# Kernel tuning notes

Measured on AMD Instinct MI355X. Metric: run time of the kernel, lower is better.

The kernel has to match this reference:

```python
import jax, jax.numpy as jnp
import numpy as np

# ---- static config (matches init_kwargs) ----
B, S, D = 2, 4096, 1024          # batch, seq_len, dim_input
L, ST = 512, 64                  # segment_len, state_len
H = 8                            # num_heads
DK0, DV0, DK1, DV1 = 64, 64, 64, 64  # per-head key/value dims for 2 memory levels
DH = 4096                        # dim_hidden (MLP)
T = 2 * ST + L                   # tokens per segment block: [state, segment, state]


def setup_inputs() -> dict:
    key = jax.random.key(0)
    ks = jax.random.split(key, 18)
    f32 = jnp.float32
    def w(k, shape, fan_in):
        return (jax.random.normal(k, shape, dtype=f32) / np.float32(np.sqrt(fan_in)))
    return {
        "x": jax.random.normal(ks[0], (B, S, D), dtype=f32),
        "state_init": 0.02 * jax.random.normal(ks[1], (ST, D), dtype=f32),
        # level-0 projections: dim_input -> per-head (key/value)
        "Wq0": w(ks[2], (D, H, DK0), D),
        "Wk0": w(ks[3], (D, H, DK0), D),
        "Wv0": w(ks[4], (D, H, DV0), D),
        # level-1 projections: level-0 value dim -> per-head (key/value)
        "Wq1": w(ks[5], (H, DV0, DK1), DV0),
        "Wk1": w(ks[6], (H, DV0, DK1), DV0),
        "Wv1": w(ks[7], (H, DV0, DV1), DV0),
        # output projection back to dim_input
        "Wo": w(ks[8], (H, DV1, D), H * DV1),
        "bo": jnp.zeros((D,), f32),
        "g_attn": jnp.ones((D,), f32),
        "b_attn": jnp.zeros((D,), f32),
        "W1": w(ks[9], (D, DH), D),
        "b1": jnp.zeros((DH,), f32),
        "W2": w(ks[10], (DH, D), DH),
        "b2": jnp.zeros((D,), f32),
        "g_mlp": jnp.ones((D,), f32),
        "b_mlp": jnp.zeros((D,), f32),
    }


def _layernorm(x, g, b, eps=1e-5):
    mu = jnp.mean(x, axis=-1, keepdims=True)
    var = jnp.mean(jnp.square(x - mu), axis=-1, keepdims=True)
    return (x - mu) * jax.lax.rsqrt(var + eps) * g + b


def _rope(x, pos):
    # x: (B, H, T, dk); rotary embedding with base 10000
    dk = x.shape[-1]
    inv_freq = jnp.power(jnp.float32(10000.0), -jnp.arange(0, dk, 2, dtype=jnp.float32) / dk)
    ang = pos[:, None] * inv_freq[None, :]              # (T, dk/2)
    cos, sin = jnp.cos(ang), jnp.sin(ang)
    x1, x2 = x[..., 0::2], x[..., 1::2]
    r1 = x1 * cos - x2 * sin
    r2 = x1 * sin + x2 * cos
    return jnp.stack([r1, r2], axis=-1).reshape(x.shape)


def _attend(q, k, v, mask):
    # q,k: (B,H,T,dk); v: (B,H,T,dv); causal mask (T,T)
    scale = jnp.float32(1.0 / np.sqrt(q.shape[-1]))
    scores = jnp.einsum('bhqc,bhkc->bhqk', q, k) * scale
    scores = jnp.where(mask, scores, jnp.float32(-1e30))
    p = jax.nn.softmax(scores, axis=-1)
    return jnp.einsum('bhqk,bhkv->bhqv', p, v)


def _remmtas(x, state_init, Wq0, Wk0, Wv0, Wq1, Wk1, Wv1, Wo, bo):
    b, s, d = x.shape
    n_seg = s // L
    xs = x.reshape(b, n_seg, L, d).transpose(1, 0, 2, 3)   # (n_seg, B, L, D)
    mask = jnp.tril(jnp.ones((T, T), dtype=bool))
    pos = jnp.arange(T, dtype=jnp.float32)
    state0 = jnp.broadcast_to(state_init, (b, ST, d))

    def step(state, seg):
        toks = jnp.concatenate([state, seg, state], axis=1)      # (B, T, D)
        # memory level 0
        q0 = _rope(jnp.einsum('btd,dhk->bhtk', toks, Wq0), pos)
        k0 = _rope(jnp.einsum('btd,dhk->bhtk', toks, Wk0), pos)
        v0 = jnp.einsum('btd,dhv->bhtv', toks, Wv0)
        o0 = _attend(q0, k0, v0, mask)                           # (B,H,T,DV0)
        # memory level 1 (consumes level-0 values, per-head)
        q1 = _rope(jnp.einsum('bhtv,hvk->bhtk', o0, Wq1), pos)
        k1 = _rope(jnp.einsum('bhtv,hvk->bhtk', o0, Wk1), pos)
        v1 = jnp.einsum('bhtv,hvw->bhtw', o0, Wv1)
        o1 = _attend(q1, k1, v1, mask)                           # (B,H,T,DV1)
        out = jnp.einsum('bhtv,hvd->btd', o1, Wo) + bo           # (B,T,D)
        new_state = out[:, ST + L:]                              # trailing state tokens
        return new_state, out[:, ST:ST + L]                      # segment output

    _, outs = jax.lax.scan(step, state0, xs)                     # (n_seg, B, L, D)
    return outs.transpose(1, 0, 2, 3).reshape(b, s, d)


def reference(x, state_init, Wq0, Wk0, Wv0, Wq1, Wk1, Wv1, Wo, bo,
              g_attn, b_attn, W1, b1, W2, b2, g_mlp, b_mlp):
    a = _remmtas(x, state_init, Wq0, Wk0, Wv0, Wq1, Wk1, Wv1, Wo, bo)
    h = _layernorm(a + x, g_attn, b_attn)
    m = jax.nn.gelu(h @ W1 + b1, approximate=False) @ W2 + b2
    # note: second residual adds the ORIGINAL x, per the source code
    return _layernorm(m + x, g_mlp, b_mlp)
```

## Files before the change

### kernel.cpp

```cpp
#include <hip/hip_runtime.h>
#include <hip/hip_bf16.h>

typedef __hip_bfloat16 bf16;
typedef short bf16x8 __attribute__((ext_vector_type(8)));
typedef float f32x4 __attribute__((ext_vector_type(4)));

#define CB 2
#define CS 4096
#define CD 1024
#define CL 512
#define CST 64
#define CH 8
#define CT 640
#define CDH 4096
#define NSEG 8
#define MCH 2048
#define LP 80

__device__ __forceinline__ float tof(float x) { return x; }
__device__ __forceinline__ float tof(bf16 x) { return __bfloat162float(x); }
__device__ __forceinline__ void storev(float* p, float v) { *p = v; }
__device__ __forceinline__ void storev(bf16* p, float v) { *p = __float2bfloat16(v); }

__device__ __forceinline__ float ldin(const void* p, size_t i, int f32w) {
    if (f32w) return ((const float*)p)[i];
    return __bfloat162float(((const bf16*)p)[i]);
}

__global__ void sniff_kernel(const void* x, int* flag) {
    if (threadIdx.x == 0 && blockIdx.x == 0) {
        const bf16* hb = (const bf16*)x;
        int plaus = 0;
        for (int i = 0; i < 256; ++i) {
            float v = __bfloat162float(hb[2 * i]);
            float a = fabsf(v);
            if (v == 0.f || (a > 1e-4f && a < 100.f)) ++plaus;
        }
        flag[0] = (plaus < 128) ? 1 : 0;
    }
}

__global__ __launch_bounds__(256) void transpose_kernel(
    const void* __restrict__ in, bf16* __restrict__ out, int R, int C,
    const int* __restrict__ flag)
{
    const int f32w = flag[0];
    __shared__ short t[64][72];
    int tid = threadIdx.x;
    int c0 = blockIdx.x * 64, r0 = blockIdx.y * 64;
    int cc = tid & 63, rr = tid >> 6;
#pragma unroll
    for (int i = 0; i < 16; ++i) {
        bf16 v = __float2bfloat16(ldin(in, (size_t)(r0 + rr + i * 4) * C + c0 + cc, f32w));
        t[rr + i * 4][cc] = *(short*)&v;
    }
    __syncthreads();
#pragma unroll
    for (int i = 0; i < 16; ++i)
        ((short*)out)[(size_t)(c0 + rr + i * 4) * R + r0 + cc] = t[cc][rr + i * 4];
}

__global__ __launch_bounds__(256) void transpose3_kernel(
    const void* __restrict__ in0, const void* __restrict__ in1, const void* __restrict__ in2,
    bf16* __restrict__ out0, bf16* __restrict__ out1, bf16* __restrict__ out2,
    const int* __restrict__ flag)
{
    const int f32w = flag[0];
    const void* in = (blockIdx.z == 0) ? in0 : (blockIdx.z == 1 ? in1 : in2);
    bf16* out = (blockIdx.z == 0) ? out0 : (blockIdx.z == 1 ? out1 : out2);
    const int R = CD, C = 512;
    __shared__ short t[64][72];
    int tid = threadIdx.x;
    int c0 = blockIdx.x * 64, r0 = blockIdx.y * 64;
    int cc = tid & 63, rr = tid >> 6;
#pragma unroll
    for (int i = 0; i < 16; ++i) {
        bf16 v = __float2bfloat16(ldin(in, (size_t)(r0 + rr + i * 4) * C + c0 + cc, f32w));
        t[rr + i * 4][cc] = *(short*)&v;
    }
    __syncthreads();
#pragma unroll
    for (int i = 0; i < 16; ++i)
        ((short*)out)[(size_t)(c0 + rr + i * 4) * R + r0 + cc] = t[cc][rr + i * 4];
}

__global__ __launch_bounds__(256) void transposeH_kernel(
    const void* __restrict__ Wq1, const void* __restrict__ Wk1, const void* __restrict__ Wv1,
    bf16* __restrict__ oq, bf16* __restrict__ ok, bf16* __restrict__ ov,
    const int* __restrict__ flag)
{
    const int f32w = flag[0];
    int which = blockIdx.x >> 3, hh = blockIdx.x & 7;
    const void* in = (which == 0) ? Wq1 : (which == 1) ? Wk1 : Wv1;
    bf16* out = (which == 0) ? oq : (which == 1) ? ok : ov;
    __shared__ short t[64][72];
    int tid = threadIdx.x;
    int cc = tid & 63, rr = tid >> 6;
    size_t base = (size_t)hh * 4096;
#pragma unroll
    for (int i = 0; i < 16; ++i) {
        bf16 v = __float2bfloat16(ldin(in, base + (size_t)(rr + i * 4) * 64 + cc, f32w));
        t[rr + i * 4][cc] = *(short*)&v;
    }
    __syncthreads();
#pragma unroll
    for (int i = 0; i < 16; ++i)
        ((short*)out)[base + (size_t)(rr + i * 4) * 64 + cc] = t[cc][rr + i * 4];
}

template <typename TC, int ACT, int OUTM>
__global__ __launch_bounds__(256) void mfma_lds(
    const bf16* __restrict__ A,
    const bf16* __restrict__ Bt0, const bf16* __restrict__ Bt1, const bf16* __restrict__ Bt2,
    TC* __restrict__ C0, TC* __restrict__ C1, TC* __restrict__ C2,
    const void* __restrict__ bias, int M, int N, int K, int seg,
    const int* __restrict__ flag)
{
    const int f32w = flag[0];
    const bf16* Bt = (blockIdx.z == 0) ? Bt0 : (blockIdx.z == 1 ? Bt1 : Bt2);
    TC* C = (blockIdx.z == 0) ? C0 : (blockIdx.z == 1 ? C1 : C2);

    __shared__ __align__(16) short As[128 * 64];
    __shared__ __align__(16) short Bs[128 * 64];

    const int tid = threadIdx.x;
    const int lane = tid & 63;
    const int w = tid >> 6;
    const int wm = w >> 1, wn = w & 1;
    const int bm = blockIdx.x * 128, bn = blockIdx.y * 128;

    f32x4 acc[4][4];
#pragma unroll
    for (int i = 0; i < 4; ++i)
#pragma unroll
        for (int j = 0; j < 4; ++j) acc[i][j] = (f32x4){0.f, 0.f, 0.f, 0.f};

    int srow[4], skc[4];
#pragma unroll
    for (int i = 0; i < 4; ++i) {
        int c = i * 256 + tid;
        srow[i] = c >> 3;
        skc[i] = (c & 7) * 8;
    }

    bf16x8 rA0[4], rB0[4], rA1[4], rB1[4];
#pragma unroll
    for (int i = 0; i < 4; ++i) {
        rA0[i] = *(const bf16x8*)(A + (size_t)(bm + srow[i]) * K + skc[i]);
        rB0[i] = *(const bf16x8*)(Bt + (size_t)(bn + srow[i]) * K + skc[i]);
        rA1[i] = *(const bf16x8*)(A + (size_t)(bm + srow[i]) * K + 64 + skc[i]);
        rB1[i] = *(const bf16x8*)(Bt + (size_t)(bn + srow[i]) * K + 64 + skc[i]);
    }

#define MFMA_PHASE                                                              \
    _Pragma("unroll")                                                           \
    for (int kh = 0; kh < 2; ++kh) {                                            \
        bf16x8 av[4], bv[4];                                                    \
        _Pragma("unroll")                                                       \
        for (int mi = 0; mi < 4; ++mi) {                                        \
            int r = wm * 64 + mi * 16 + (lane & 15);                            \
            int cl = kh * 4 + (lane >> 4);                                      \
            av[mi] = *(const bf16x8*)&As[r * 64 + cl * 8];                      \
        }                                                                       \
        _Pragma("unroll")                                                       \
        for (int nj = 0; nj < 4; ++nj) {                                        \
            int r = wn * 64 + nj * 16 + (lane & 15);                            \
            int cl = kh * 4 + (lane >> 4);                                      \
            bv[nj] = *(const bf16x8*)&Bs[r * 64 + cl * 8];                      \
        }                                                                       \
        _Pragma("unroll")                                                       \
        for (int mi = 0; mi < 4; ++mi)                                          \
            _Pragma("unroll")                                                   \
            for (int nj = 0; nj < 4; ++nj)                                      \
                acc[mi][nj] = __builtin_amdgcn_mfma_f32_16x16x32_bf16(          \
                    av[mi], bv[nj], acc[mi][nj], 0, 0, 0);                      \
    }

    for (int k0 = 0; k0 < K; k0 += 128) {
        __syncthreads();
#pragma unroll
        for (int i = 0; i < 4; ++i) {
            *(bf16x8*)&As[(size_t)(i * 256 + tid) * 8] = rA0[i];
            *(bf16x8*)&Bs[(size_t)(i * 256 + tid) * 8] = rB0[i];
        }
        if (k0 + 128 < K) {
            int kn = k0 + 128;
#pragma unroll
            for (int i = 0; i < 4; ++i) {
                rA0[i] = *(const bf16x8*)(A + (size_t)(bm + srow[i]) * K + kn + skc[i]);
                rB0[i] = *(const bf16x8*)(Bt + (size_t)(bn + srow[i]) * K + kn + skc[i]);
            }
        }
        __syncthreads();
        MFMA_PHASE

        __syncthreads();
#pragma unroll
        for (int i = 0; i < 4; ++i) {
            *(bf16x8*)&As[(size_t)(i * 256 + tid) * 8] = rA1[i];
            *(bf16x8*)&Bs[(size_t)(i * 256 + tid) * 8] = rB1[i];
        }
        if (k0 + 192 < K) {
            int kn = k0 + 192;
#pragma unroll
            for (int i = 0; i < 4; ++i) {
                rA1[i] = *(const bf16x8*)(A + (size_t)(bm + srow[i]) * K + kn + skc[i]);
                rB1[i] = *(const bf16x8*)(Bt + (size_t)(bn + srow[i]) * K + kn + skc[i]);
            }
        }
        __syncthreads();
        MFMA_PHASE
    }
#undef MFMA_PHASE

#pragma unroll
    for (int mi = 0; mi < 4; ++mi) {
#pragma unroll
        for (int nj = 0; nj < 4; ++nj) {
            int c = bn + wn * 64 + nj * 16 + (lane & 15);
            float bia = bias ? ldin(bias, c, f32w) : 0.f;
#pragma unroll
            for (int r = 0; r < 4; ++r) {
                int row = bm + wm * 64 + mi * 16 + (lane >> 4) * 4 + r;
                float v = acc[mi][nj][r] + bia;
                if (ACT == 1) v = 0.5f * v * (1.0f + erff(v * 0.70710678118654752f));
                if (OUTM == 0) {
                    storev(C + (size_t)row * N + c, v);
                } else {
                    int bb2 = row / CT, t = row % CT;
                    if (t >= CST) {
                        if (t < CST + CL)
                            storev(C0 + ((size_t)bb2 * CS + (size_t)seg * CL + (t - CST)) * CD + c, v);
                        else
                            storev(C1 + ((size_t)bb2 * CST + (t - CST - CL)) * CD + c, v);
                    }
                }
            }
        }
    }
}

__global__ __launch_bounds__(256) void ropeV_kernel(
    bf16* __restrict__ q, bf16* __restrict__ k,
    const bf16* __restrict__ v, bf16* __restrict__ vt)
{
    int t0 = blockIdx.x * 64, hh = blockIdx.y, b = blockIdx.z;
    int tid = threadIdx.x;
    __shared__ short lt[64][72];
    int c = tid & 63;
    int r0 = tid >> 6;
    int ip = c >> 1;
    float inv = powf(10000.f, -(float)(2 * ip) / 64.f);
#pragma unroll
    for (int i = 0; i < 16; ++i) {
        int r = r0 + i * 4;
        int t = t0 + r;
        size_t idx = ((size_t)b * CT + t) * 512 + hh * 64 + c;
        float qv = tof(q[idx]);
        float kv = tof(k[idx]);
        float ang = (float)t * inv;
        float sn, cs;
        sincosf(ang, &sn, &cs);
        float qp = __shfl_xor(qv, 1);
        float kp = __shfl_xor(kv, 1);
        float rq, rk;
        if (c & 1) { rq = qp * sn + qv * cs; rk = kp * sn + kv * cs; }
        else       { rq = qv * cs - qp * sn; rk = kv * cs - kp * sn; }
        q[idx] = __float2bfloat16(rq);
        k[idx] = __float2bfloat16(rk);
        lt[r][c] = ((const short*)v)[idx];
    }
    __syncthreads();
#pragma unroll
    for (int i = 0; i < 16; ++i) {
        int c2 = r0 + i * 4;
        int r2 = c;
        ((short*)vt)[((size_t)(b * CH + hh) * 64 + c2) * CT + t0 + r2] = lt[r2][c2];
    }
}

template <int FUSE>
__global__ __launch_bounds__(256) void attn_mfma(
    const bf16* __restrict__ q, const bf16* __restrict__ k, const bf16* __restrict__ vt,
    bf16* __restrict__ o,
    int qsb, int qsh, int qst,
    int ksb, int ksh, int kst,
    int ob, int oh, int ot,
    const bf16* __restrict__ Wq1t, const bf16* __restrict__ Wk1t, const bf16* __restrict__ Wv1t,
    bf16* __restrict__ q1o, bf16* __restrict__ k1o, bf16* __restrict__ v1to)
{
    const int tid = threadIdx.x;
    const int lane = tid & 63;
    const int wrow = tid >> 6;
    const int hh = blockIdx.y, b = blockIdx.z;
    const int qbase = ((int)gridDim.x - 1 - (int)blockIdx.x) * 64;

    __shared__ __align__(16) short Qs[64 * LP];
    __shared__ __align__(16) short Ks[64 * LP];
    __shared__ __align__(16) short Vs[64 * LP];
    __shared__ __align__(16) short Ps[64 * LP];

    const size_t qb0 = (size_t)b * qsb + (size_t)hh * qsh;
    const size_t kb0 = (size_t)b * ksb + (size_t)hh * ksh;
    const size_t vtb = (size_t)(b * CH + hh) * 64 * CT;

    int srow[2], skc[2], soff[2];
#pragma unroll
    for (int i = 0; i < 2; ++i) {
        int c = i * 256 + tid;
        srow[i] = c >> 3;
        skc[i] = c & 7;
        soff[i] = srow[i] * LP + skc[i] * 8;
    }

    bf16x8 rQ[2], rK[2], rV[2];
#pragma unroll
    for (int i = 0; i < 2; ++i) {
        rQ[i] = *(const bf16x8*)(q + qb0 + (size_t)(qbase + srow[i]) * qst + skc[i] * 8);
        rK[i] = *(const bf16x8*)(k + kb0 + (size_t)srow[i] * kst + skc[i] * 8);
        rV[i] = *(const bf16x8*)(vt + vtb + (size_t)srow[i] * CT + skc[i] * 8);
    }

    float mrow[4], lrow[4];
    f32x4 oacc[4];
#pragma unroll
    for (int r = 0; r < 4; ++r) { mrow[r] = -1e30f; lrow[r] = 0.f; }
#pragma unroll
    for (int nd = 0; nd < 4; ++nd) oacc[nd] = (f32x4){0.f, 0.f, 0.f, 0.f};

    const int ntiles = qbase / 64 + 1;
    for (int ti = 0; ti < ntiles; ++ti) {
        __syncthreads();
        if (ti == 0) {
#pragma unroll
            for (int i = 0; i < 2; ++i) *(bf16x8*)&Qs[soff[i]] = rQ[i];
        }
#pragma unroll
        for (int i = 0; i < 2; ++i) {
            *(bf16x8*)&Ks[soff[i]] = rK[i];
            *(bf16x8*)&Vs[soff[i]] = rV[i];
        }
        if (ti + 1 < ntiles) {
            int j1 = (ti + 1) * 64;
#pragma unroll
            for (int i = 0; i < 2; ++i) {
                rK[i] = *(const bf16x8*)(k + kb0 + (size_t)(j1 + srow[i]) * kst + skc[i] * 8);
                rV[i] = *(const bf16x8*)(vt + vtb + (size_t)srow[i] * CT + j1 + skc[i] * 8);
            }
        }
        __syncthreads();

        f32x4 sacc[4];
#pragma unroll
        for (int nj = 0; nj < 4; ++nj) sacc[nj] = (f32x4){0.f, 0.f, 0.f, 0.f};
#pragma unroll
        for (int kh = 0; kh < 2; ++kh) {
            int cl = kh * 4 + (lane >> 4);
            bf16x8 av = *(const bf16x8*)&Qs[(wrow * 16 + (lane & 15)) * LP + cl * 8];
#pragma unroll
            for (int nj = 0; nj < 4; ++nj) {
                bf16x8 bv = *(const bf16x8*)&Ks[(nj * 16 + (lane & 15)) * LP + cl * 8];
                sacc[nj] = __builtin_amdgcn_mfma_f32_16x16x32_bf16(av, bv, sacc[nj], 0, 0, 0);
            }
        }

        const bool diag = (ti == ntiles - 1);
        float pm[4] = {-1e30f, -1e30f, -1e30f, -1e30f};
#pragma unroll
        for (int nj = 0; nj < 4; ++nj) {
            int col_l = nj * 16 + (lane & 15);
#pragma unroll
            for (int r = 0; r < 4; ++r) {
                int row_l = wrow * 16 + ((lane >> 4) << 2) + r;
                float s = (diag && col_l > row_l) ? -1e30f : sacc[nj][r] * 0.125f;
                sacc[nj][r] = s;
                pm[r] = fmaxf(pm[r], s);
            }
        }
#pragma unroll
        for (int msk = 1; msk < 16; msk <<= 1)
#pragma unroll
            for (int r = 0; r < 4; ++r) pm[r] = fmaxf(pm[r], __shfl_xor(pm[r], msk));

        float corr[4], rs[4] = {0.f, 0.f, 0.f, 0.f};
#pragma unroll
        for (int r = 0; r < 4; ++r) {
            float mn = fmaxf(mrow[r], pm[r]);
            corr[r] = __expf(mrow[r] - mn);
            mrow[r] = mn;
        }
#pragma unroll
        for (int nj = 0; nj < 4; ++nj)
#pragma unroll
            for (int r = 0; r < 4; ++r) {
                float p = __expf(sacc[nj][r] - mrow[r]);
                sacc[nj][r] = p;
                rs[r] += p;
            }
#pragma unroll
        for (int msk = 1; msk < 16; msk <<= 1)
#pragma unroll
            for (int r = 0; r < 4; ++r) rs[r] += __shfl_xor(rs[r], msk);
#pragma unroll
        for (int r = 0; r < 4; ++r) lrow[r] = lrow[r] * corr[r] + rs[r];
#pragma unroll
        for (int nd = 0; nd < 4; ++nd)
#pragma unroll
            for (int r = 0; r < 4; ++r) oacc[nd][r] *= corr[r];

#pragma unroll
        for (int nj = 0; nj < 4; ++nj)
#pragma unroll
            for (int r = 0; r < 4; ++r) {
                bf16 pb = __float2bfloat16(sacc[nj][r]);
                Ps[(wrow * 16 + ((lane >> 4) << 2) + r) * LP + nj * 16 + (lane & 15)] =
                    *(short*)&pb;
            }

#pragma unroll
        for (int kh = 0; kh < 2; ++kh) {
            int cl = kh * 4 + (lane >> 4);
            bf16x8 pa = *(const bf16x8*)&Ps[(wrow * 16 + (lane & 15)) * LP + cl * 8];
#pragma unroll
            for (int nd = 0; nd < 4; ++nd) {
                bf16x8 bv = *(const bf16x8*)&Vs[(nd * 16 + (lane & 15)) * LP + cl * 8];
                oacc[nd] = __builtin_amdgcn_mfma_f32_16x16x32_bf16(pa, bv, oacc[nd], 0, 0, 0);
            }
        }
    }

    if (FUSE == 0) {
#pragma unroll
        for (int nd = 0; nd < 4; ++nd) {
#pragma unroll
            for (int r = 0; r < 4; ++r) {
                int row_g = qbase + wrow * 16 + ((lane >> 4) << 2) + r;
                int col = nd * 16 + (lane & 15);
                storev(&o[(size_t)b * ob + (size_t)hh * oh + (size_t)row_g * ot + col],
                       oacc[nd][r] / lrow[r]);
            }
        }
    } else {
#pragma unroll
        for (int nd = 0; nd < 4; ++nd)
#pragma unroll
            for (int r = 0; r < 4; ++r) {
                int row_l = wrow * 16 + ((lane >> 4) << 2) + r;
                bf16 ob16 = __float2bfloat16(oacc[nd][r] / lrow[r]);
                Qs[row_l * LP + nd * 16 + (lane & 15)] = *(short*)&ob16;
            }
        __syncthreads();

        const size_t whb = (size_t)hh * 4096;
        f32x4 qa[4], ka[4], va[4];
#pragma unroll
        for (int nj = 0; nj < 4; ++nj) {
            qa[nj] = (f32x4){0.f, 0.f, 0.f, 0.f};
            ka[nj] = (f32x4){0.f, 0.f, 0.f, 0.f};
            va[nj] = (f32x4){0.f, 0.f, 0.f, 0.f};
        }
#pragma unroll
        for (int kh = 0; kh < 2; ++kh) {
            int cl = kh * 4 + (lane >> 4);
            bf16x8 av = *(const bf16x8*)&Qs[(wrow * 16 + (lane & 15)) * LP + cl * 8];
#pragma unroll
            for (int nj = 0; nj < 4; ++nj) {
                int rowb = nj * 16 + (lane & 15);
                bf16x8 bq = *(const bf16x8*)(Wq1t + whb + (size_t)rowb * 64 + cl * 8);
                bf16x8 bk = *(const bf16x8*)(Wk1t + whb + (size_t)rowb * 64 + cl * 8);
                bf16x8 bw = *(const bf16x8*)(Wv1t + whb + (size_t)rowb * 64 + cl * 8);
                qa[nj] = __builtin_amdgcn_mfma_f32_16x16x32_bf16(av, bq, qa[nj], 0, 0, 0);
                ka[nj] = __builtin_amdgcn_mfma_f32_16x16x32_bf16(av, bk, ka[nj], 0, 0, 0);
                va[nj] = __builtin_amdgcn_mfma_f32_16x16x32_bf16(av, bw, va[nj], 0, 0, 0);
            }
        }
        const size_t bh = (size_t)(b * CH + hh);
#pragma unroll
        for (int nj = 0; nj < 4; ++nj) {
            int col = nj * 16 + (lane & 15);
            int ip = col >> 1;
            float inv = powf(10000.f, -(float)(2 * ip) / 64.f);
#pragma unroll
            for (int r = 0; r < 4; ++r) {
                int row_l = wrow * 16 + ((lane >> 4) << 2) + r;
                int t = qbase + row_l;
                float ang = (float)t * inv;
                float sn, cs;
                sincosf(ang, &sn, &cs);
                float aq = qa[nj][r], ak = ka[nj][r];
                float pq = __shfl_xor(aq, 1);
                float pk = __shfl_xor(ak, 1);
                float rq, rk;
                if (col & 1) { rq = pq * sn + aq * cs; rk = pk * sn + ak * cs; }
                else         { rq = aq * cs - pq * sn; rk = ak * cs - pk * sn; }
                size_t roff = (bh * CT + t) * 64 + col;
                q1o[roff] = __float2bfloat16(rq);
                k1o[roff] = __float2bfloat16(rk);
                v1to[(bh * 64 + col) * CT + t] = __float2bfloat16(va[nj][r]);
            }
        }
    }
}

__global__ __launch_bounds__(256) void build_toks_kernel(
    const void* __restrict__ x, const float* __restrict__ state, bf16* __restrict__ toks,
    int seg, const int* __restrict__ flag)
{
    const int f32w = flag[0];
    int idx = blockIdx.x * 256 + threadIdx.x;
    int d = idx & (CD - 1);
    int t = (idx >> 10) % CT;
    int b = idx / (CT * CD);
    float v;
    if (t < CST) v = state[(b * CST + t) * CD + d];
    else if (t < CST + CL) v = ldin(x, ((size_t)b * CS + seg * CL + (t - CST)) * CD + d, f32w);
    else v = state[(b * CST + (t - CST - CL)) * CD + d];
    toks[idx] = __float2bfloat16(v);
}

__global__ __launch_bounds__(256) void init_state_kernel(
    const void* __restrict__ s0, float* __restrict__ state, const int* __restrict__ flag)
{
    const int f32w = flag[0];
    int idx = blockIdx.x * 256 + threadIdx.x;
    state[idx] = ldin(s0, idx % (CST * CD), f32w);
}

__global__ __launch_bounds__(256) void ln_kernel(
    const float* __restrict__ ra, const void* __restrict__ x,
    const void* __restrict__ g, const void* __restrict__ bb,
    void* __restrict__ outp, int out_ext, const int* __restrict__ flag)
{
    const int f32w = flag[0];
    int row = blockIdx.x;
    int tid = threadIdx.x;
    __shared__ float buf[CD];
    __shared__ float red[4];

    float s = 0.f;
    for (int c = tid; c < CD; c += 256) {
        float v = ra[(size_t)row * CD + c] + ldin(x, (size_t)row * CD + c, f32w);
        buf[c] = v;
        s += v;
    }
#pragma unroll
    for (int off = 32; off; off >>= 1) s += __shfl_xor(s, off);
    if ((tid & 63) == 0) red[tid >> 6] = s;
    __syncthreads();
    float mu = (red[0] + red[1] + red[2] + red[3]) * (1.f / CD);
    __syncthreads();

    float vs = 0.f;
    for (int c = tid; c < CD; c += 256) {
        float d0 = buf[c] - mu;
        vs += d0 * d0;
    }
#pragma unroll
    for (int off = 32; off; off >>= 1) vs += __shfl_xor(vs, off);
    if ((tid & 63) == 0) red[tid >> 6] = vs;
    __syncthreads();
    float var = (red[0] + red[1] + red[2] + red[3]) * (1.f / CD);
    float rs = rsqrtf(var + 1e-5f);

    for (int c = tid; c < CD; c += 256) {
        float y = (buf[c] - mu) * rs * ldin(g, c, f32w) + ldin(bb, c, f32w);
        size_t idx = (size_t)row * CD + c;
        if (!out_ext) {
            ((bf16*)outp)[idx] = __float2bfloat16(y);
        } else if (f32w) {
            ((float*)outp)[idx] = y;
        } else {
            ((bf16*)outp)[idx] = __float2bfloat16(y);
        }
    }
}

extern "C" void kernel_launch(void* const* d_in, const int* in_sizes, int n_in,
                              void* d_out, int out_size, void* d_ws, size_t ws_size,
                              hipStream_t stream)
{
    const void* x      = d_in[0];
    const void* s0     = d_in[1];
    const void* Wq0    = d_in[2];
    const void* Wk0    = d_in[3];
    const void* Wv0    = d_in[4];
    const void* Wq1    = d_in[5];
    const void* Wk1    = d_in[6];
    const void* Wv1    = d_in[7];
    const void* Wo     = d_in[8];
    const void* bo     = d_in[9];
    const void* g_attn = d_in[10];
    const void* b_attn = d_in[11];
    const void* W1     = d_in[12];
    const void* b1     = d_in[13];
    const void* W2     = d_in[14];
    const void* b2     = d_in[15];
    const void* g_mlp  = d_in[16];
    const void* b_mlp  = d_in[17];

    int* flag = (int*)d_ws;
    float* f = (float*)((char*)d_ws + 16);
    float* toks_slot = f; f += (size_t)CB * CT * CD;
    float* q0_slot = f;  f += (size_t)CB * CH * CT * 64;
    float* k0_slot = f;  f += (size_t)CB * CH * CT * 64;
    float* v0_slot = f;  f += (size_t)CB * CH * CT * 64;
    float* o0_slot = f;  f += (size_t)CB * CH * CT * 64;
    float* q1_slot = f;  f += (size_t)CB * CH * CT * 64;
    float* k1_slot = f;  f += (size_t)CB * CH * CT * 64;
    float* v1_slot = f;  f += (size_t)CB * CH * CT * 64;
    float* o1t_slot = f; f += (size_t)CB * CT * (CH * 64);
    float* seg_slot = f; f += (size_t)CB * CT * CD;
    float* state = f;   f += (size_t)CB * CST * CD;
    float* a = f;       f += (size_t)CB * CS * CD;
    bf16* h = (bf16*)f;
    bf16* tail = h + (size_t)CB * CS * CD;

    bf16* toks = (bf16*)toks_slot;
    bf16* q0b = (bf16*)q0_slot;
    bf16* k0b = (bf16*)k0_slot;
    bf16* v0b = (bf16*)v0_slot;
    bf16* v0t = (bf16*)o0_slot;
    bf16* q1b = (bf16*)q1_slot;
    bf16* k1b = (bf16*)k1_slot;
    bf16* v1t = (bf16*)v1_slot;
    bf16* o1t = (bf16*)o1t_slot;
    bf16* WtQ = h;
    bf16* WtK = WtQ + (size_t)512 * 1024;
    bf16* WtV = WtK + (size_t)512 * 1024;
    bf16* WtO = WtV + (size_t)512 * 1024;
    bf16* WtQ1 = WtO + (size_t)1024 * 512;
    bf16* WtK1 = WtQ1 + (size_t)8 * 4096;
    bf16* WtV1 = WtK1 + (size_t)8 * 4096;
    bf16* g1  = (bf16*)toks_slot;
    bf16* Wt1 = g1 + (size_t)MCH * CDH;
    bf16* Wt2 = tail;

    sniff_kernel<<<1, 64, 0, stream>>>(x, flag);
    init_state_kernel<<<(CB * CST * CD) / 256, 256, 0, stream>>>(s0, state, flag);

    transpose3_kernel<<<dim3(8, 16, 3), 256, 0, stream>>>(
        Wq0, Wk0, Wv0, WtQ, WtK, WtV, flag);
    transpose_kernel<<<dim3(16, 8), 256, 0, stream>>>(Wo, WtO, 512, CD, flag);
    transposeH_kernel<<<24, 256, 0, stream>>>(Wq1, Wk1, Wv1, WtQ1, WtK1, WtV1, flag);

    for (int seg = 0; seg < NSEG; ++seg) {
        build_toks_kernel<<<(CB * CT * CD) / 256, 256, 0, stream>>>(x, state, toks, seg, flag);
        mfma_lds<bf16, 0, 0><<<dim3(10, 4, 3), 256, 0, stream>>>(
            toks, WtQ, WtK, WtV, q0b, k0b, v0b, nullptr, CB * CT, 512, CD, 0, flag);
        ropeV_kernel<<<dim3(CT / 64, CH, CB), 256, 0, stream>>>(q0b, k0b, v0b, v0t);
        attn_mfma<1><<<dim3(CT / 64, CH, CB), 256, 0, stream>>>(
            q0b, k0b, v0t, nullptr,
            CT * 512, 64, 512,
            CT * 512, 64, 512,
            0, 0, 0,
            WtQ1, WtK1, WtV1, q1b, k1b, v1t);
        attn_mfma<0><<<dim3(CT / 64, CH, CB), 256, 0, stream>>>(
            q1b, k1b, v1t, o1t,
            CH * CT * 64, CT * 64, 64,
            CH * CT * 64, CT * 64, 64,
            CT * 512, 64, 512,
            nullptr, nullptr, nullptr, nullptr, nullptr, nullptr);
        mfma_lds<float, 0, 1><<<dim3(10, 8, 1), 256, 0, stream>>>(
            o1t, WtO, WtO, WtO, a, state, a, bo, CB * CT, CD, 512, seg, flag);
    }

    ln_kernel<<<CB * CS, 256, 0, stream>>>(a, x, g_attn, b_attn, h, 0, flag);

    transpose_kernel<<<dim3(CDH / 64, CD / 64), 256, 0, stream>>>(W1, Wt1, CD, CDH, flag);
    transpose_kernel<<<dim3(CD / 64, CDH / 64), 256, 0, stream>>>(W2, Wt2, CDH, CD, flag);

    for (int c = 0; c < (CB * CS) / MCH; ++c) {
        mfma_lds<bf16, 1, 0><<<dim3(MCH / 128, CDH / 128, 1), 256, 0, stream>>>(
            h + (size_t)c * MCH * CD, Wt1, Wt1, Wt1, g1, g1, g1, b1, MCH, CDH, CD, 0, flag);
        mfma_lds<float, 0, 0><<<dim3(MCH / 128, CD / 128, 1), 256, 0, stream>>>(
            g1, Wt2, Wt2, Wt2,
            a + (size_t)c * MCH * CD, a + (size_t)c * MCH * CD, a + (size_t)c * MCH * CD,
            b2, MCH, CD, CDH, 0, flag);
    }
    ln_kernel<<<CB * CS, 256, 0, stream>>>(a, x, g_mlp, b_mlp, d_out, 1, flag);
}
```

Baseline: 1.311 ms.

## Split MLP over hidden dimension with accumulating second GEMM for full-grid launches

The MLP is now chunked along the hidden dimension instead of along rows. Each chunk computes a 1024-wide slice of the GELU activations for all 8192 rows, then the second GEMM multiplies it by the matching K-slice of W2 and accumulates into the fp32 output. The GEMM kernel gains lda/ldb strides, a bias offset and an accumulate mode to support this. The aim is that every MLP launch fills the GPU with 512 blocks instead of 128 for the down projection. In exchange, the fp32 output is read and rewritten several extra times.

```diff
diff --git a/kernel.cpp b/kernel.cpp
--- a/kernel.cpp
+++ b/kernel.cpp
@@ -14,7 +14,6 @@
 #define CT 640
 #define CDH 4096
 #define NSEG 8
-#define MCH 2048
 #define LP 80
 
 __device__ __forceinline__ float tof(float x) { return x; }
@@ -108,12 +107,13 @@
         ((short*)out)[base + (size_t)(rr + i * 4) * 64 + cc] = t[cc][rr + i * 4];
 }
 
-template <typename TC, int ACT, int OUTM>
+template <typename TC, int ACT, int OUTM, int ACCUM>
 __global__ __launch_bounds__(256) void mfma_lds(
     const bf16* __restrict__ A,
     const bf16* __restrict__ Bt0, const bf16* __restrict__ Bt1, const bf16* __restrict__ Bt2,
     TC* __restrict__ C0, TC* __restrict__ C1, TC* __restrict__ C2,
-    const void* __restrict__ bias, int M, int N, int K, int seg,
+    const void* __restrict__ bias, int boff,
+    int M, int N, int K, int lda, int ldb, int seg,
     const int* __restrict__ flag)
 {
     const int f32w = flag[0];
@@ -146,10 +146,10 @@
     bf16x8 rA0[4], rB0[4], rA1[4], rB1[4];
 #pragma unroll
     for (int i = 0; i < 4; ++i) {
-        rA0[i] = *(const bf16x8*)(A + (size_t)(bm + srow[i]) * K + skc[i]);
-        rB0[i] = *(const bf16x8*)(Bt + (size_t)(bn + srow[i]) * K + skc[i]);
-        rA1[i] = *(const bf16x8*)(A + (size_t)(bm + srow[i]) * K + 64 + skc[i]);
-        rB1[i] = *(const bf16x8*)(Bt + (size_t)(bn + srow[i]) * K + 64 + skc[i]);
+        rA0[i] = *(const bf16x8*)(A + (size_t)(bm + srow[i]) * lda + skc[i]);
+        rB0[i] = *(const bf16x8*)(Bt + (size_t)(bn + srow[i]) * ldb + skc[i]);
+        rA1[i] = *(const bf16x8*)(A + (size_t)(bm + srow[i]) * lda + 64 + skc[i]);
+        rB1[i] = *(const bf16x8*)(Bt + (size_t)(bn + srow[i]) * ldb + 64 + skc[i]);
     }
 
 #define MFMA_PHASE                                                              \
@@ -187,8 +187,8 @@
             int kn = k0 + 128;
 #pragma unroll
             for (int i = 0; i < 4; ++i) {
-                rA0[i] = *(const bf16x8*)(A + (size_t)(bm + srow[i]) * K + kn + skc[i]);
-                rB0[i] = *(const bf16x8*)(Bt + (size_t)(bn + srow[i]) * K + kn + skc[i]);
+                rA0[i] = *(const bf16x8*)(A + (size_t)(bm + srow[i]) * lda + kn + skc[i]);
+                rB0[i] = *(const bf16x8*)(Bt + (size_t)(bn + srow[i]) * ldb + kn + skc[i]);
             }
         }
         __syncthreads();
@@ -204,8 +204,8 @@
             int kn = k0 + 192;
 #pragma unroll
             for (int i = 0; i < 4; ++i) {
-                rA1[i] = *(const bf16x8*)(A + (size_t)(bm + srow[i]) * K + kn + skc[i]);
-                rB1[i] = *(const bf16x8*)(Bt + (size_t)(bn + srow[i]) * K + kn + skc[i]);
+                rA1[i] = *(const bf16x8*)(A + (size_t)(bm + srow[i]) * lda + kn + skc[i]);
+                rB1[i] = *(const bf16x8*)(Bt + (size_t)(bn + srow[i]) * ldb + kn + skc[i]);
             }
         }
         __syncthreads();
@@ -218,13 +218,14 @@
 #pragma unroll
         for (int nj = 0; nj < 4; ++nj) {
             int c = bn + wn * 64 + nj * 16 + (lane & 15);
-            float bia = bias ? ldin(bias, c, f32w) : 0.f;
+            float bia = bias ? ldin(bias, boff + c, f32w) : 0.f;
 #pragma unroll
             for (int r = 0; r < 4; ++r) {
                 int row = bm + wm * 64 + mi * 16 + (lane >> 4) * 4 + r;
                 float v = acc[mi][nj][r] + bia;
                 if (ACT == 1) v = 0.5f * v * (1.0f + erff(v * 0.70710678118654752f));
                 if (OUTM == 0) {
+                    if (ACCUM) v += tof(C[(size_t)row * N + c]);
                     storev(C + (size_t)row * N + c, v);
                 } else {
                     int bb2 = row / CT, t = row % CT;
@@ -632,7 +633,7 @@
     bf16* WtK1 = WtQ1 + (size_t)8 * 4096;
     bf16* WtV1 = WtK1 + (size_t)8 * 4096;
     bf16* g1  = (bf16*)toks_slot;
-    bf16* Wt1 = g1 + (size_t)MCH * CDH;
+    bf16* Wt1 = g1 + (size_t)CB * CS * CD;
     bf16* Wt2 = tail;
 
     sniff_kernel<<<1, 64, 0, stream>>>(x, flag);
@@ -645,8 +646,9 @@
 
     for (int seg = 0; seg < NSEG; ++seg) {
         build_toks_kernel<<<(CB * CT * CD) / 256, 256, 0, stream>>>(x, state, toks, seg, flag);
-        mfma_lds<bf16, 0, 0><<<dim3(10, 4, 3), 256, 0, stream>>>(
-            toks, WtQ, WtK, WtV, q0b, k0b, v0b, nullptr, CB * CT, 512, CD, 0, flag);
+        mfma_lds<bf16, 0, 0, 0><<<dim3(10, 4, 3), 256, 0, stream>>>(
+            toks, WtQ, WtK, WtV, q0b, k0b, v0b, nullptr, 0,
+            CB * CT, 512, CD, CD, CD, 0, flag);
         ropeV_kernel<<<dim3(CT / 64, CH, CB), 256, 0, stream>>>(q0b, k0b, v0b, v0t);
         attn_mfma<1><<<dim3(CT / 64, CH, CB), 256, 0, stream>>>(
             q0b, k0b, v0t, nullptr,
@@ -660,8 +662,9 @@
             CH * CT * 64, CT * 64, 64,
             CT * 512, 64, 512,
             nullptr, nullptr, nullptr, nullptr, nullptr, nullptr);
-        mfma_lds<float, 0, 1><<<dim3(10, 8, 1), 256, 0, stream>>>(
-            o1t, WtO, WtO, WtO, a, state, a, bo, CB * CT, CD, 512, seg, flag);
+        mfma_lds<float, 0, 1, 0><<<dim3(10, 8, 1), 256, 0, stream>>>(
+            o1t, WtO, WtO, WtO, a, state, a, bo, 0,
+            CB * CT, CD, 512, 512, 512, seg, flag);
     }
 
     ln_kernel<<<CB * CS, 256, 0, stream>>>(a, x, g_attn, b_attn, h, 0, flag);
@@ -669,13 +672,18 @@
     transpose_kernel<<<dim3(CDH / 64, CD / 64), 256, 0, stream>>>(W1, Wt1, CD, CDH, flag);
     transpose_kernel<<<dim3(CD / 64, CDH / 64), 256, 0, stream>>>(W2, Wt2, CDH, CD, flag);
 
-    for (int c = 0; c < (CB * CS) / MCH; ++c) {
-        mfma_lds<bf16, 1, 0><<<dim3(MCH / 128, CDH / 128, 1), 256, 0, stream>>>(
-            h + (size_t)c * MCH * CD, Wt1, Wt1, Wt1, g1, g1, g1, b1, MCH, CDH, CD, 0, flag);
-        mfma_lds<float, 0, 0><<<dim3(MCH / 128, CD / 128, 1), 256, 0, stream>>>(
-            g1, Wt2, Wt2, Wt2,
-            a + (size_t)c * MCH * CD, a + (size_t)c * MCH * CD, a + (size_t)c * MCH * CD,
-            b2, MCH, CD, CDH, 0, flag);
+    for (int c = 0; c < 4; ++c) {
+        mfma_lds<bf16, 1, 0, 0><<<dim3(64, 8, 1), 256, 0, stream>>>(
+            h, Wt1 + (size_t)c * 1024 * CD, Wt1, Wt1, g1, g1, g1,
+            b1, c * 1024, CB * CS, 1024, CD, CD, CD, 0, flag);
+        if (c == 0)
+            mfma_lds<float, 0, 0, 0><<<dim3(64, 8, 1), 256, 0, stream>>>(
+                g1, Wt2 + (size_t)c * 1024, Wt2, Wt2, a, a, a,
+                b2, 0, CB * CS, CD, 1024, 1024, CDH, 0, flag);
+        else
+            mfma_lds<float, 0, 0, 1><<<dim3(64, 8, 1), 256, 0, stream>>>(
+                g1, Wt2 + (size_t)c * 1024, Wt2, Wt2, a, a, a,
+                nullptr, 0, CB * CS, CD, 1024, 1024, CDH, 0, flag);
     }
     ln_kernel<<<CB * CS, 256, 0, stream>>>(a, x, g_mlp, b_mlp, d_out, 1, flag);
 }
```

After: 1.214 ms. 1.08x faster.
